# Optimization experiments

Measured on AMD Instinct MI355X. Metric: run time of the kernel, lower is better.

## Reference

```python
import jax, jax.numpy as jnp
import numpy as np

EMB_SIZE = 200000
DIM = 256
WALK_LEN = 80
WINDOW = 5
BATCH = 32
NEGATIVE = 5
NEG_WEIGHT = 1.0
LR = 0.025
LAP_NORM = 0.01


def _pos_index():
    # replicates init_emb2pos_index: for each center i, u-index = context j, v-index = center i
    us, vs = [], []
    for i in range(WALK_LEN):
        for j in range(max(0, i - WINDOW), i):
            us.append(j); vs.append(i)
        for j in range(i + 1, min(WALK_LEN, i + 1 + WINDOW)):
            us.append(j); vs.append(i)
    us = np.asarray(us, np.int32)
    vs = np.asarray(vs, np.int32)
    off = (np.arange(BATCH, dtype=np.int32) * WALK_LEN)[:, None]
    return (us[None, :] + off).reshape(-1), (vs[None, :] + off).reshape(-1)


def _neg_index(pos_v):
    # replicates init_emb2neg_index: u-index = center repeated NEGATIVE times per positive pair;
    # v-index = shuffled node positions from the whole batch (in-batch negatives)
    negu = np.repeat(pos_v, NEGATIVE)
    negv = np.tile(np.arange(BATCH * WALK_LEN, dtype=np.int32), NEGATIVE * WINDOW * 2)
    rng = np.random.default_rng(0)
    rng.shuffle(negv)
    return negu, negv[: len(negu)]


def setup_inputs() -> dict:
    key = jax.random.key(0)
    k1, k2, k3 = jax.random.split(key, 3)
    initrange = 1.0 / DIM
    u_weight = jax.random.uniform(k1, (EMB_SIZE, DIM), jnp.float32, -initrange, initrange)
    # original inits v to zero; use small noise so scores/grads are non-degenerate for testing
    v_weight = 0.01 * jax.random.normal(k2, (EMB_SIZE, DIM), jnp.float32)
    # sigmoid lookup table: torch.sigmoid(torch.arange(-6.01, 6.01, 0.01)) -> 1202 entries
    table = jax.nn.sigmoid(jnp.arange(1202, dtype=jnp.float32) * 0.01 - 6.01)
    table = table.at[0].set(0.0).at[-1].set(1.0)
    nodes = jax.random.randint(k3, (BATCH, WALK_LEN), 0, EMB_SIZE, dtype=jnp.int32)
    pu, pv = _pos_index()
    nu, nv = _neg_index(pv)
    return {
        "nodes": nodes,
        "u_weight": u_weight,
        "v_weight": v_weight,
        "lookup_table": table,
        "idx_posu": jnp.asarray(pu),
        "idx_posv": jnp.asarray(pv),
        "idx_negu": jnp.asarray(nu),
        "idx_negv": jnp.asarray(nv),
    }


def reference(nodes, u_weight, v_weight, lookup_table, idx_posu, idx_posv, idx_negu, idx_negv):
    flat = nodes.reshape(-1)                       # [B*L]
    emb_u = u_weight[flat]                         # [B*L, D]
    emb_v = v_weight[flat]                         # [B*L, D]

    def fast_sigmoid(s):
        idx = jnp.floor((s + 6.01) / 0.01).astype(jnp.int32)
        return lookup_table[idx]

    # positive pairs
    epu = emb_u[idx_posu]                          # [P, D]
    epv = emb_v[idx_posv]
    pos = jnp.clip(jnp.sum(epu * epv, axis=1), -6.0, 6.0)
    s = (1.0 - fast_sigmoid(pos))[:, None]
    gu_pos = s * epv + LAP_NORM * (epv - epu)
    gv_pos = s * epu + LAP_NORM * (epu - epv)
    grad_u = jnp.zeros_like(emb_u).at[idx_posu].add(gu_pos)
    grad_v = jnp.zeros_like(emb_v).at[idx_posv].add(gv_pos)

    # in-batch negative pairs
    enu = emb_u[idx_negu]                          # [P*neg, D]
    env = emb_v[idx_negv]
    neg = jnp.clip(jnp.sum(enu * env, axis=1), -6.0, 6.0)
    ns = (-fast_sigmoid(neg))[:, None]
    grad_u = grad_u.at[idx_negu].add(NEG_WEIGHT * ns * env)
    grad_v = grad_v.at[idx_negv].add(NEG_WEIGHT * ns * enu)

    # fused SGD scatter-update of the embedding tables
    new_u = u_weight.at[flat].add(LR * grad_u)
    new_v = v_weight.at[flat].add(LR * grad_v)
    return jnp.concatenate([new_u, new_v], axis=0)  # [2*EMB_SIZE, D]
```

## Files before the change

kernel.cpp:

```cpp
#include <hip/hip_runtime.h>

#define EMB      200000
#define DIM      256
#define WALK     80
#define WIN      5
#define BATCH    32
#define PPW      770
#define NPOSN    (BATCH * PPW)
#define NNEG     (NPOSN * 5)
#define NPOSIT   (BATCH * WALK)
#define LR       0.025f
#define LAP      0.01f
#define INV_STRIDE 64

#define GRAD_BLOCKS 1280
#define COPY_BLOCKS 2048

__device__ __forceinline__ float wave_sum(float s) {
#pragma unroll
    for (int off = 32; off > 0; off >>= 1) s += __shfl_xor(s, off, 64);
    return s;
}

__device__ __forceinline__ float fast_sig(const float* __restrict__ t, float d) {
    float s = fminf(fmaxf(d, -6.0f), 6.0f);
    int idx = (int)floorf((s + 6.01f) / 0.01f);
    return t[idx];
}

__global__ void k_gather(const int* __restrict__ nodes,
                         const float* __restrict__ uw,
                         const float* __restrict__ vw,
                         float* __restrict__ eu,
                         float* __restrict__ ev,
                         int* __restrict__ cnt) {
    int p = blockIdx.x;
    int d = threadIdx.x;
    int node = nodes[p];
    eu[p * DIM + d] = uw[(size_t)node * DIM + d];
    ev[p * DIM + d] = vw[(size_t)node * DIM + d];
    if (d == 0) cnt[p] = 0;
}

__global__ void k_inv(const int* __restrict__ negv,
                      int* __restrict__ cnt,
                      int* __restrict__ inv) {
    int m = blockIdx.x * blockDim.x + threadIdx.x;
    if (m >= NNEG) return;
    int p = negv[m];
    int slot = atomicAdd(&cnt[p], 1);
    inv[p * INV_STRIDE + slot] = m;
}

__global__ void __launch_bounds__(256) k_fused(
        const float* __restrict__ uw,
        const float* __restrict__ vw,
        const float* __restrict__ table,
        const int*   __restrict__ negu,
        const int*   __restrict__ negv,
        const float* __restrict__ eu,
        const float* __restrict__ ev,
        const int*   __restrict__ cnt,
        const int*   __restrict__ inv,
        float*       __restrict__ gu,
        float*       __restrict__ gv,
        float*       __restrict__ out) {
    if (blockIdx.x >= GRAD_BLOCKS) {
        const size_t T4 = (size_t)EMB * DIM / 4;
        int cb  = blockIdx.x - GRAD_BLOCKS;
        int tbl = cb & 1;
        int blk = cb >> 1;
        const float4* __restrict__ src = tbl ? (const float4*)vw : (const float4*)uw;
        float4* __restrict__ dst = (float4*)out + (size_t)tbl * T4;
        const size_t stride = (size_t)(COPY_BLOCKS / 2) * 256;
        for (size_t i = (size_t)blk * 256 + threadIdx.x; i < T4; i += stride)
            dst[i] = src[i];
        return;
    }

    int wid  = blockIdx.x * 4 + (threadIdx.x >> 6);
    int lane = threadIdx.x & 63;
    int side = wid >= NPOSIT;
    int p    = side ? wid - NPOSIT : wid;
    int b    = p / WALK;
    int i    = p - b * WALK;

    int jlo = (i - WIN < 0) ? 0 : i - WIN;
    int jhi = (i + WIN > WALK - 1) ? WALK - 1 : i + WIN;

    if (!side) {
        const float4 mu = *(const float4*)&eu[p * DIM + lane * 4];
        float gx = 0.f, gy = 0.f, gz = 0.f, gw = 0.f;

        for (int j = jlo; j <= jhi; ++j) {
            if (j == i) continue;
            int q = b * WALK + j;
            float4 qv = *(const float4*)&ev[q * DIM + lane * 4];
            float d1 = wave_sum(mu.x * qv.x + mu.y * qv.y + mu.z * qv.z + mu.w * qv.w);
            float s1 = 1.0f - fast_sig(table, d1);
            gx += s1 * qv.x + LAP * (qv.x - mu.x);
            gy += s1 * qv.y + LAP * (qv.y - mu.y);
            gz += s1 * qv.z + LAP * (qv.z - mu.z);
            gw += s1 * qv.w + LAP * (qv.w - mu.w);
        }

        int S = 0;
        for (int k = 0; k < i; ++k)
            S += (k < WIN ? k : WIN) + ((WALK - 1 - k) < WIN ? (WALK - 1 - k) : WIN);
        int ci = (i < WIN ? i : WIN) + ((WALK - 1 - i) < WIN ? (WALK - 1 - i) : WIN);
        int mstart = 5 * (PPW * b + S);
        int mcnt   = 5 * ci;
        for (int t = 0; t < mcnt; ++t) {
            int z = negv[mstart + t];
            float4 zv = *(const float4*)&ev[z * DIM + lane * 4];
            float d  = wave_sum(mu.x * zv.x + mu.y * zv.y + mu.z * zv.z + mu.w * zv.w);
            float ns = -fast_sig(table, d);
            gx += ns * zv.x; gy += ns * zv.y; gz += ns * zv.z; gw += ns * zv.w;
        }
        *(float4*)&gu[p * DIM + lane * 4] = make_float4(gx, gy, gz, gw);
    } else {
        const float4 mv = *(const float4*)&ev[p * DIM + lane * 4];
        float gx = 0.f, gy = 0.f, gz = 0.f, gw = 0.f;

        for (int j = jlo; j <= jhi; ++j) {
            if (j == i) continue;
            int q = b * WALK + j;
            float4 qu = *(const float4*)&eu[q * DIM + lane * 4];
            float d2 = wave_sum(qu.x * mv.x + qu.y * mv.y + qu.z * mv.z + qu.w * mv.w);
            float s2 = 1.0f - fast_sig(table, d2);
            gx += s2 * qu.x + LAP * (qu.x - mv.x);
            gy += s2 * qu.y + LAP * (qu.y - mv.y);
            gz += s2 * qu.z + LAP * (qu.z - mv.z);
            gw += s2 * qu.w + LAP * (qu.w - mv.w);
        }

        int ninv = cnt[p];
        for (int t = 0; t < ninv; ++t) {
            int m = inv[p * INV_STRIDE + t];
            int a = negu[m];
            float4 au = *(const float4*)&eu[a * DIM + lane * 4];
            float d  = wave_sum(au.x * mv.x + au.y * mv.y + au.z * mv.z + au.w * mv.w);
            float ns = -fast_sig(table, d);
            gx += ns * au.x; gy += ns * au.y; gz += ns * au.z; gw += ns * au.w;
        }
        *(float4*)&gv[p * DIM + lane * 4] = make_float4(gx, gy, gz, gw);
    }
}

__global__ void k_apply(const int* __restrict__ nodes,
                        const float* __restrict__ gu,
                        const float* __restrict__ gv,
                        float* __restrict__ out) {
    int p = blockIdx.x;
    int d = threadIdx.x;
    int node = nodes[p];
    atomicAdd(&out[(size_t)node * DIM + d],               LR * gu[p * DIM + d]);
    atomicAdd(&out[((size_t)EMB + (size_t)node) * DIM + d], LR * gv[p * DIM + d]);
}

extern "C" void kernel_launch(void* const* d_in, const int* in_sizes, int n_in,
                              void* d_out, int out_size, void* d_ws, size_t ws_size,
                              hipStream_t stream) {
    const int*   nodes = (const int*)d_in[0];
    const float* uw    = (const float*)d_in[1];
    const float* vw    = (const float*)d_in[2];
    const float* table = (const float*)d_in[3];
    const int*   negu  = (const int*)d_in[6];
    const int*   negv  = (const int*)d_in[7];
    float* out = (float*)d_out;

    float* eu  = (float*)d_ws;
    float* ev  = eu + (size_t)NPOSIT * DIM;
    float* gu  = ev + (size_t)NPOSIT * DIM;
    float* gv  = gu + (size_t)NPOSIT * DIM;
    int*   cnt = (int*)(gv + (size_t)NPOSIT * DIM);
    int*   inv = cnt + NPOSIT;

    k_gather<<<NPOSIT, DIM, 0, stream>>>(nodes, uw, vw, eu, ev, cnt);
    k_inv<<<(NNEG + 255) / 256, 256, 0, stream>>>(negv, cnt, inv);
    k_fused<<<GRAD_BLOCKS + COPY_BLOCKS, 256, 0, stream>>>(
        uw, vw, table, negu, negv, eu, ev, cnt, inv, gu, gv, out);
    k_apply<<<NPOSIT, DIM, 0, stream>>>(nodes, gu, gv, out);
}
```

Before: 214.8 us.

## Dedupe node updates via owner map and stream table copy with nontemporal ops

Drops the staging gather kernel: the gradient kernel reads embedding rows straight from the weight tables through `nodes`. Per-position gradients go into per-owner accumulators via atomics, where the owner is the first position holding the same node. A final kernel then writes `weight + LR*acc` directly instead of doing atomic adds into the output. The bulk table copy moves into its own kernel using nontemporal loads and stores. The aim is to cut the gather traffic and the output atomics and to speed the copy, at the cost of no longer overlapping the copy with gradient work and adding a memset plus a serial owner search.

Measured after the change: 365.5 us. 70.2% more time.

```diff
diff --git a/kernel.cpp b/kernel.cpp
--- a/kernel.cpp
+++ b/kernel.cpp
@@ -6,15 +6,18 @@
 #define WIN      5
 #define BATCH    32
 #define PPW      770
-#define NPOSN    (BATCH * PPW)
-#define NNEG     (NPOSN * 5)
-#define NPOSIT   (BATCH * WALK)
+#define NNEG     123200
+#define NPOSIT   2560
 #define LR       0.025f
 #define LAP      0.01f
 #define INV_STRIDE 64
 
+#define INV_BLOCKS  482
+#define OWN_BLOCKS  10
 #define GRAD_BLOCKS 1280
 #define COPY_BLOCKS 2048
+
+typedef __attribute__((ext_vector_type(4))) float v4f;
 
 __device__ __forceinline__ float wave_sum(float s) {
 #pragma unroll
@@ -28,74 +31,62 @@
     return t[idx];
 }
 
-__global__ void k_gather(const int* __restrict__ nodes,
-                         const float* __restrict__ uw,
-                         const float* __restrict__ vw,
-                         float* __restrict__ eu,
-                         float* __restrict__ ev,
-                         int* __restrict__ cnt) {
-    int p = blockIdx.x;
-    int d = threadIdx.x;
-    int node = nodes[p];
-    eu[p * DIM + d] = uw[(size_t)node * DIM + d];
-    ev[p * DIM + d] = vw[(size_t)node * DIM + d];
-    if (d == 0) cnt[p] = 0;
-}
-
-__global__ void k_inv(const int* __restrict__ negv,
-                      int* __restrict__ cnt,
-                      int* __restrict__ inv) {
-    int m = blockIdx.x * blockDim.x + threadIdx.x;
-    if (m >= NNEG) return;
-    int p = negv[m];
-    int slot = atomicAdd(&cnt[p], 1);
-    inv[p * INV_STRIDE + slot] = m;
-}
-
-__global__ void __launch_bounds__(256) k_fused(
+__global__ void k_prep(const int* __restrict__ negv,
+                       const int* __restrict__ nodes,
+                       int* __restrict__ cnt,
+                       int* __restrict__ inv,
+                       int* __restrict__ owner) {
+    int bid = blockIdx.x;
+    if (bid < INV_BLOCKS) {
+        int m = bid * 256 + threadIdx.x;
+        if (m < NNEG) {
+            int p = negv[m];
+            int slot = atomicAdd(&cnt[p], 1);
+            inv[p * INV_STRIDE + slot] = m;
+        }
+    } else {
+        int p = (bid - INV_BLOCKS) * 256 + threadIdx.x;
+        if (p < NPOSIT) {
+            int n = nodes[p];
+            int j = 0;
+            while (nodes[j] != n) ++j;
+            owner[p] = j;
+        }
+    }
+}
+
+__global__ void __launch_bounds__(256) k_grad(
+        const int*   __restrict__ nodes,
         const float* __restrict__ uw,
         const float* __restrict__ vw,
         const float* __restrict__ table,
         const int*   __restrict__ negu,
         const int*   __restrict__ negv,
-        const float* __restrict__ eu,
-        const float* __restrict__ ev,
         const int*   __restrict__ cnt,
         const int*   __restrict__ inv,
-        float*       __restrict__ gu,
-        float*       __restrict__ gv,
-        float*       __restrict__ out) {
-    if (blockIdx.x >= GRAD_BLOCKS) {
-        const size_t T4 = (size_t)EMB * DIM / 4;
-        int cb  = blockIdx.x - GRAD_BLOCKS;
-        int tbl = cb & 1;
-        int blk = cb >> 1;
-        const float4* __restrict__ src = tbl ? (const float4*)vw : (const float4*)uw;
-        float4* __restrict__ dst = (float4*)out + (size_t)tbl * T4;
-        const size_t stride = (size_t)(COPY_BLOCKS / 2) * 256;
-        for (size_t i = (size_t)blk * 256 + threadIdx.x; i < T4; i += stride)
-            dst[i] = src[i];
-        return;
-    }
-
+        const int*   __restrict__ owner,
+        float*       __restrict__ accu,
+        float*       __restrict__ accv) {
     int wid  = blockIdx.x * 4 + (threadIdx.x >> 6);
     int lane = threadIdx.x & 63;
     int side = wid >= NPOSIT;
     int p    = side ? wid - NPOSIT : wid;
     int b    = p / WALK;
     int i    = p - b * WALK;
+    int col  = lane * 4;
 
     int jlo = (i - WIN < 0) ? 0 : i - WIN;
     int jhi = (i + WIN > WALK - 1) ? WALK - 1 : i + WIN;
+    int node_p = nodes[p];
 
     if (!side) {
-        const float4 mu = *(const float4*)&eu[p * DIM + lane * 4];
+        const float4 mu = *(const float4*)&uw[(size_t)node_p * DIM + col];
         float gx = 0.f, gy = 0.f, gz = 0.f, gw = 0.f;
 
         for (int j = jlo; j <= jhi; ++j) {
             if (j == i) continue;
             int q = b * WALK + j;
-            float4 qv = *(const float4*)&ev[q * DIM + lane * 4];
+            float4 qv = *(const float4*)&vw[(size_t)nodes[q] * DIM + col];
             float d1 = wave_sum(mu.x * qv.x + mu.y * qv.y + mu.z * qv.z + mu.w * qv.w);
             float s1 = 1.0f - fast_sig(table, d1);
             gx += s1 * qv.x + LAP * (qv.x - mu.x);
@@ -112,20 +103,25 @@
         int mcnt   = 5 * ci;
         for (int t = 0; t < mcnt; ++t) {
             int z = negv[mstart + t];
-            float4 zv = *(const float4*)&ev[z * DIM + lane * 4];
+            float4 zv = *(const float4*)&vw[(size_t)nodes[z] * DIM + col];
             float d  = wave_sum(mu.x * zv.x + mu.y * zv.y + mu.z * zv.z + mu.w * zv.w);
             float ns = -fast_sig(table, d);
             gx += ns * zv.x; gy += ns * zv.y; gz += ns * zv.z; gw += ns * zv.w;
         }
-        *(float4*)&gu[p * DIM + lane * 4] = make_float4(gx, gy, gz, gw);
+
+        float* dst = &accu[(size_t)owner[p] * DIM + col];
+        atomicAdd(dst + 0, gx);
+        atomicAdd(dst + 1, gy);
+        atomicAdd(dst + 2, gz);
+        atomicAdd(dst + 3, gw);
     } else {
-        const float4 mv = *(const float4*)&ev[p * DIM + lane * 4];
+        const float4 mv = *(const float4*)&vw[(size_t)node_p * DIM + col];
         float gx = 0.f, gy = 0.f, gz = 0.f, gw = 0.f;
 
         for (int j = jlo; j <= jhi; ++j) {
             if (j == i) continue;
             int q = b * WALK + j;
-            float4 qu = *(const float4*)&eu[q * DIM + lane * 4];
+            float4 qu = *(const float4*)&uw[(size_t)nodes[q] * DIM + col];
             float d2 = wave_sum(qu.x * mv.x + qu.y * mv.y + qu.z * mv.z + qu.w * mv.w);
             float s2 = 1.0f - fast_sig(table, d2);
             gx += s2 * qu.x + LAP * (qu.x - mv.x);
@@ -138,24 +134,50 @@
         for (int t = 0; t < ninv; ++t) {
             int m = inv[p * INV_STRIDE + t];
             int a = negu[m];
-            float4 au = *(const float4*)&eu[a * DIM + lane * 4];
+            float4 au = *(const float4*)&uw[(size_t)nodes[a] * DIM + col];
             float d  = wave_sum(au.x * mv.x + au.y * mv.y + au.z * mv.z + au.w * mv.w);
             float ns = -fast_sig(table, d);
             gx += ns * au.x; gy += ns * au.y; gz += ns * au.z; gw += ns * au.w;
         }
-        *(float4*)&gv[p * DIM + lane * 4] = make_float4(gx, gy, gz, gw);
+
+        float* dst = &accv[(size_t)owner[p] * DIM + col];
+        atomicAdd(dst + 0, gx);
+        atomicAdd(dst + 1, gy);
+        atomicAdd(dst + 2, gz);
+        atomicAdd(dst + 3, gw);
     }
 }
 
-__global__ void k_apply(const int* __restrict__ nodes,
-                        const float* __restrict__ gu,
-                        const float* __restrict__ gv,
+__global__ void __launch_bounds__(256) k_copy(const float* __restrict__ uw,
+                                              const float* __restrict__ vw,
+                                              float* __restrict__ out) {
+    const size_t T4 = (size_t)EMB * DIM / 4;
+    int cb  = blockIdx.x;
+    int tbl = cb & 1;
+    size_t blk = (size_t)(cb >> 1);
+    const v4f* __restrict__ src = (const v4f*)(tbl ? vw : uw);
+    v4f* __restrict__ dst = (v4f*)out + (size_t)tbl * T4;
+    const size_t stride = (size_t)(COPY_BLOCKS / 2) * 256;
+    for (size_t i = blk * 256 + threadIdx.x; i < T4; i += stride) {
+        v4f v = __builtin_nontemporal_load(&src[i]);
+        __builtin_nontemporal_store(v, &dst[i]);
+    }
+}
+
+__global__ void k_final(const int* __restrict__ nodes,
+                        const float* __restrict__ uw,
+                        const float* __restrict__ vw,
+                        const float* __restrict__ accu,
+                        const float* __restrict__ accv,
+                        const int* __restrict__ owner,
                         float* __restrict__ out) {
     int p = blockIdx.x;
+    if (owner[p] != p) return;
     int d = threadIdx.x;
-    int node = nodes[p];
-    atomicAdd(&out[(size_t)node * DIM + d],               LR * gu[p * DIM + d]);
-    atomicAdd(&out[((size_t)EMB + (size_t)node) * DIM + d], LR * gv[p * DIM + d]);
+    int n = nodes[p];
+    size_t off = (size_t)n * DIM + d;
+    out[off] = uw[off] + LR * accu[(size_t)p * DIM + d];
+    out[(size_t)EMB * DIM + off] = vw[off] + LR * accv[(size_t)p * DIM + d];
 }
 
 extern "C" void kernel_launch(void* const* d_in, const int* in_sizes, int n_in,
@@ -169,16 +191,18 @@
     const int*   negv  = (const int*)d_in[7];
     float* out = (float*)d_out;
 
-    float* eu  = (float*)d_ws;
-    float* ev  = eu + (size_t)NPOSIT * DIM;
-    float* gu  = ev + (size_t)NPOSIT * DIM;
-    float* gv  = gu + (size_t)NPOSIT * DIM;
-    int*   cnt = (int*)(gv + (size_t)NPOSIT * DIM);
-    int*   inv = cnt + NPOSIT;
-
-    k_gather<<<NPOSIT, DIM, 0, stream>>>(nodes, uw, vw, eu, ev, cnt);
-    k_inv<<<(NNEG + 255) / 256, 256, 0, stream>>>(negv, cnt, inv);
-    k_fused<<<GRAD_BLOCKS + COPY_BLOCKS, 256, 0, stream>>>(
-        uw, vw, table, negu, negv, eu, ev, cnt, inv, gu, gv, out);
-    k_apply<<<NPOSIT, DIM, 0, stream>>>(nodes, gu, gv, out);
-}
+    int*   cnt   = (int*)d_ws;
+    float* accu  = (float*)(cnt + NPOSIT);
+    float* accv  = accu + (size_t)NPOSIT * DIM;
+    int*   inv   = (int*)(accv + (size_t)NPOSIT * DIM);
+    int*   owner = inv + (size_t)NPOSIT * INV_STRIDE;
+
+    const size_t zero_bytes = (size_t)NPOSIT * 4 + 2 * (size_t)NPOSIT * DIM * 4;
+    hipMemsetAsync(d_ws, 0, zero_bytes, stream);
+
+    k_prep<<<INV_BLOCKS + OWN_BLOCKS, 256, 0, stream>>>(negv, nodes, cnt, inv, owner);
+    k_grad<<<GRAD_BLOCKS, 256, 0, stream>>>(nodes, uw, vw, table, negu, negv,
+                                            cnt, inv, owner, accu, accv);
+    k_copy<<<COPY_BLOCKS, 256, 0, stream>>>(uw, vw, out);
+    k_final<<<NPOSIT, DIM, 0, stream>>>(nodes, uw, vw, accu, accv, owner, out);
+}
```
